# Kernel optimization log

Measured on AMD Instinct MI355X. Metric: run time of the kernel, lower is better.

The kernel has to match this reference:

```python
import jax, jax.numpy as jnp
import numpy as np

N_NODES = 200_000
N_EDGES = 6_400_000
N_GRAPHS = 512
F_IN = 92   # CGCNN atom feature dim
WIDTH = 10  # hard-coded config.width in GCNSimple
F_OUT = 1   # output_features


def setup_inputs() -> dict:
    key = jax.random.key(0)
    ks = jax.random.split(key, 10)
    atom_features = jax.random.normal(ks[0], (N_NODES, F_IN), dtype=jnp.float32)
    r = jax.random.normal(ks[1], (N_EDGES, 3), dtype=jnp.float32)
    W_emb = jax.random.normal(ks[2], (F_IN, WIDTH), dtype=jnp.float32) * 0.1
    b_emb = jax.random.normal(ks[3], (WIDTH,), dtype=jnp.float32) * 0.1
    W1 = jax.random.normal(ks[4], (WIDTH, WIDTH), dtype=jnp.float32) * 0.3
    b1 = jax.random.normal(ks[5], (WIDTH,), dtype=jnp.float32) * 0.1
    W2 = jax.random.normal(ks[6], (WIDTH, F_OUT), dtype=jnp.float32) * 0.3
    b2 = jax.random.normal(ks[7], (F_OUT,), dtype=jnp.float32) * 0.1
    src = jax.random.randint(ks[8], (N_EDGES,), 0, N_NODES, dtype=jnp.int32)
    dst = jax.random.randint(ks[9], (N_EDGES,), 0, N_NODES, dtype=jnp.int32)
    graph_ids = jnp.sort(jax.random.randint(jax.random.fold_in(key, 99), (N_NODES,), 0, N_GRAPHS, dtype=jnp.int32))
    return {
        "atom_features": atom_features, "r": r,
        "W_emb": W_emb, "b_emb": b_emb, "W1": W1, "b1": b1, "W2": W2, "b2": b2,
        "src": src, "dst": dst, "graph_ids": graph_ids, "num_graphs": N_GRAPHS,
    }


def reference(atom_features, r, W_emb, b_emb, W1, b1, W2, b2, src, dst, graph_ids, num_graphs):
    n = atom_features.shape[0]
    dt = atom_features.dtype
    # edge weights: exp(-||r||^2 / lengthscale^2), lengthscale = 1
    ew = jnp.exp(-jnp.sum(r * r, axis=1))  # [E]

    # unweighted degrees (DGL GraphConv norm='both' ignores edge_weight in norm)
    out_deg = jnp.clip(jnp.zeros(n, dt).at[src].add(1.0), 1.0)
    in_deg = jnp.clip(jnp.zeros(n, dt).at[dst].add(1.0), 1.0)
    inv_sqrt_out = out_deg ** -0.5
    inv_sqrt_in = in_deg ** -0.5

    def gconv(x, W, b, mm_first):
        # DGL GraphConv, norm='both': scale by src deg, weighted-sum aggregate,
        # scale by dst deg; weight applied before aggregation iff in > out.
        x = x * inv_sqrt_out[:, None]
        if mm_first:
            x = x @ W
        msg = x[src] * ew[:, None]                      # [E, d] gather
        agg = jax.ops.segment_sum(msg, dst, num_segments=n)  # [N, d] scatter-add
        if not mm_first:
            agg = agg @ W
        return agg * inv_sqrt_in[:, None] + b

    h = atom_features @ W_emb + b_emb                  # atom embedding [N, 10]
    x = jax.nn.relu(gconv(h, W1, b1, mm_first=False))  # 10 -> 10 (in == out: aggregate first)
    x = gconv(x, W2, b2, mm_first=True)                # 10 -> 1  (in > out: mm first)

    # AvgPooling: mean node feature per graph
    counts = jax.ops.segment_sum(jnp.ones(n, dt), graph_ids, num_segments=num_graphs)
    pooled = jax.ops.segment_sum(x, graph_ids, num_segments=num_graphs) / counts[:, None]
    return jnp.squeeze(pooled)  # [num_graphs]
```

## Files before the change

kernel.cpp:

```cpp
#include <hip/hip_runtime.h>
#include <math.h>

#define NNODES  200000
#define NEDGES  6400000
#define NGRAPHS 512
#define FIN     92
#define WID     10
#define HPAD    16
#define NBLK    ((NNODES + 255) / 256)

#define LBITS   10
#define LSIZE   1024
#define LMASK   (LSIZE - 1)
#define NB      196
#define SUBSH   7
#define SUBN    128
#define NSUB    1563
#define NSUBP   1608
#define PBLK    1280
#define EPB     (NEDGES / PBLK)
#define TILE    1250
#define NTILE   (EPB / TILE)
#define CELLS   (2 * NB)
#define CNT_N   (CELLS * PBLK)
#define SBLKS   (CNT_N / 256)
#define REF_GRID (NB * 8)

#define CHBITS  14
#define NCHK    13
#define SKEYS   (SUBN * NCHK)
#define SKPAD   1792
#define SKPT    7
#define SMAX    5120

#define LPN     8
#define LPNSH   3
#define NPB     (256 / LPN)
#define AGG_BLKS (NNODES / NPB)

__global__ void k_part_count(const int* __restrict__ src,
                             const int* __restrict__ dst,
                             int* __restrict__ cnt,
                             int* __restrict__ subcnt) {
    __shared__ int hSub[NSUB];
    __shared__ int hS[NB];
    int tid = threadIdx.x, k = blockIdx.x;
    for (int i = tid; i < NSUB; i += 256) hSub[i] = 0;
    if (tid < NB) hS[tid] = 0;
    __syncthreads();
    int base = k * EPB;
    for (int i = tid; i < EPB; i += 256) {
        int e = base + i;
        atomicAdd(&hSub[dst[e] >> SUBSH], 1);
        atomicAdd(&hS[src[e] >> LBITS], 1);
    }
    __syncthreads();
    if (tid < NB) {
        int s = 0;
        int b0 = tid * 8;
#pragma unroll
        for (int j = 0; j < 8; j++) {
            int ix = b0 + j;
            if (ix < NSUB) s += hSub[ix];
        }
        cnt[tid * PBLK + k] = s;
        cnt[(NB + tid) * PBLK + k] = hS[tid];
    }
    for (int i = tid; i < NSUB; i += 256) {
        int v = hSub[i];
        if (v) atomicAdd(&subcnt[i], v);
    }
}

__global__ void k_scan_partial(const int* __restrict__ cnt,
                               int* __restrict__ partial) {
    __shared__ int sdata[256];
    int tid = threadIdx.x;
    sdata[tid] = cnt[blockIdx.x * 256 + tid];
    __syncthreads();
    for (int s = 128; s > 0; s >>= 1) {
        if (tid < s) sdata[tid] += sdata[tid + s];
        __syncthreads();
    }
    if (tid == 0) partial[blockIdx.x] = sdata[0];
}

__global__ void k_scan_top(int* __restrict__ partial) {
    __shared__ int buf[1024];
    __shared__ int carry_s;
    if (threadIdx.x == 0) carry_s = 0;
    __syncthreads();
    for (int base = 0; base < SBLKS; base += 1024) {
        int i = base + threadIdx.x;
        int c = carry_s;
        int orig = (i < SBLKS) ? partial[i] : 0;
        buf[threadIdx.x] = orig;
        __syncthreads();
        for (int off = 1; off < 1024; off <<= 1) {
            int t = (threadIdx.x >= off) ? buf[threadIdx.x - off] : 0;
            __syncthreads();
            buf[threadIdx.x] += t;
            __syncthreads();
        }
        if (i < SBLKS) partial[i] = buf[threadIdx.x] - orig + c;
        __syncthreads();
        if (threadIdx.x == 0) carry_s = c + buf[1023];
        __syncthreads();
    }
}

__global__ void k_scan_apply(int* __restrict__ cnt,
                             const int* __restrict__ partial) {
    __shared__ int buf[256];
    int tid = threadIdx.x;
    int i = blockIdx.x * 256 + tid;
    int v = cnt[i];
    buf[tid] = v;
    __syncthreads();
    for (int off = 1; off < 256; off <<= 1) {
        int t = (tid >= off) ? buf[tid - off] : 0;
        __syncthreads();
        buf[tid] += t;
        __syncthreads();
    }
    cnt[i] = buf[tid] - v + partial[blockIdx.x];
}

__global__ void k_subscan(int* __restrict__ subcnt,
                          int* __restrict__ subcur) {
    __shared__ int sbuf[256];
    int tid = threadIdx.x;
    int vals[SKPT];
    int sum = 0;
#pragma unroll
    for (int j = 0; j < SKPT; j++) {
        int c = tid * SKPT + j;
        int v = (c < NSUB) ? subcnt[c] : 0;
        vals[j] = v;
        sum += v;
    }
    sbuf[tid] = sum;
    __syncthreads();
    for (int off = 1; off < 256; off <<= 1) {
        int t = (tid >= off) ? sbuf[tid - off] : 0;
        __syncthreads();
        sbuf[tid] += t;
        __syncthreads();
    }
    int run = sbuf[tid] - sum;
#pragma unroll
    for (int j = 0; j < SKPT; j++) {
        int c = tid * SKPT + j;
        if (c < NSUB) {
            subcnt[c] = run;
            subcur[c] = run;
            run += vals[j];
        }
    }
    if (tid == 0) subcnt[NSUB] = NEDGES;
}

__global__ void k_part_scatter(const float* __restrict__ r,
                               const int* __restrict__ src,
                               const int* __restrict__ dst,
                               const int* __restrict__ cnt,
                               float2* __restrict__ dstpart,
                               unsigned short* __restrict__ srcpart) {
    __shared__ int curD[NB], curS[NB];
    __shared__ int hD[NB], hS[NB];
    __shared__ int baseD[NB], baseS[NB];
    __shared__ int segD[NB], segS[NB];
    __shared__ int wsum[4];
    __shared__ float stW[TILE];
    __shared__ int   stK[TILE];
    __shared__ int   ddD[TILE];
    __shared__ unsigned short stS[TILE];
    __shared__ int   ddS[TILE];

    int tid = threadIdx.x, k = blockIdx.x;
    int lane = tid & 63, wv = tid >> 6;
    if (tid < NB) {
        curD[tid] = cnt[tid * PBLK + k];
        curS[tid] = cnt[(NB + tid) * PBLK + k] - NEDGES;
    }
    __syncthreads();

    int base = k * EPB;
    for (int t = 0; t < NTILE; t++) {
        int tbase = base + t * TILE;
        if (tid < NB) { hD[tid] = 0; hS[tid] = 0; }
        __syncthreads();
        for (int i = tid; i < TILE; i += 256) {
            int e = tbase + i;
            atomicAdd(&hD[dst[e] >> LBITS], 1);
            atomicAdd(&hS[src[e] >> LBITS], 1);
        }
        __syncthreads();
        {
            int v = (tid < NB) ? hD[tid] : 0;
            int x = v;
#pragma unroll
            for (int off = 1; off < 64; off <<= 1) {
                int tv = __shfl_up(x, off, 64);
                if (lane >= off) x += tv;
            }
            if (lane == 63) wsum[wv] = x;
            __syncthreads();
            if (tid == 0) {
                int a = 0;
#pragma unroll
                for (int wvi = 0; wvi < 4; wvi++) { int tv = wsum[wvi]; wsum[wvi] = a; a += tv; }
            }
            __syncthreads();
            int excl = x - v + wsum[wv];
            if (tid < NB) {
                baseD[tid] = excl;
                segD[tid] = curD[tid];
                curD[tid] += v;
                hD[tid] = excl;
            }
        }
        __syncthreads();
        {
            int v = (tid < NB) ? hS[tid] : 0;
            int x = v;
#pragma unroll
            for (int off = 1; off < 64; off <<= 1) {
                int tv = __shfl_up(x, off, 64);
                if (lane >= off) x += tv;
            }
            if (lane == 63) wsum[wv] = x;
            __syncthreads();
            if (tid == 0) {
                int a = 0;
#pragma unroll
                for (int wvi = 0; wvi < 4; wvi++) { int tv = wsum[wvi]; wsum[wvi] = a; a += tv; }
            }
            __syncthreads();
            int excl = x - v + wsum[wv];
            if (tid < NB) {
                baseS[tid] = excl;
                segS[tid] = curS[tid];
                curS[tid] += v;
                hS[tid] = excl;
            }
        }
        __syncthreads();
        for (int i = tid; i < TILE; i += 256) {
            int e = tbase + i;
            int s = src[e], d = dst[e];
            float x = r[3 * e + 0];
            float y = r[3 * e + 1];
            float z = r[3 * e + 2];
            float w = expf(-(x * x + y * y + z * z));
            int cd = d >> LBITS;
            int idx = atomicAdd(&hD[cd], 1);
            stW[idx] = w;
            stK[idx] = (s << LBITS) | (d & LMASK);
            ddD[idx] = segD[cd] + (idx - baseD[cd]);
            int cs = s >> LBITS;
            int ids = atomicAdd(&hS[cs], 1);
            stS[ids] = (unsigned short)(s & LMASK);
            ddS[ids] = segS[cs] + (ids - baseS[cs]);
        }
        __syncthreads();
        for (int i = tid; i < TILE; i += 256) {
            dstpart[ddD[i]] = make_float2(stW[i], __int_as_float(stK[i]));
            srcpart[ddS[i]] = stS[i];
        }
        __syncthreads();
    }
}

__global__ void k_bucket_odeg(const unsigned short* __restrict__ srcpart,
                              const int* __restrict__ cnt,
                              float* __restrict__ inv_out) {
    __shared__ int hist[LSIZE];
    int tid = threadIdx.x, b = blockIdx.x;
    int bstart = cnt[(NB + b) * PBLK] - NEDGES;
    int bend = (b == NB - 1) ? NEDGES : (cnt[(NB + b + 1) * PBLK] - NEDGES);
    for (int l = tid; l < LSIZE; l += 256) hist[l] = 0;
    __syncthreads();
    for (int p = bstart + tid; p < bend; p += 256)
        atomicAdd(&hist[srcpart[p]], 1);
    __syncthreads();
    for (int l = tid; l < LSIZE; l += 256) {
        int n = (b << LBITS) + l;
        if (n < NNODES) {
            int c = hist[l];
            inv_out[n] = rsqrtf((float)(c < 1 ? 1 : c));
        }
    }
}

__global__ void k_refine(const float2* __restrict__ dstpart,
                         const int* __restrict__ cnt,
                         int* __restrict__ subcur,
                         float2* __restrict__ dstfine) {
    int p = blockIdx.x >> 3;
    int q = blockIdx.x & 7;
    int bstart = cnt[p * PBLK];
    int bend = (p == NB - 1) ? NEDGES : cnt[(p + 1) * PBLK];
    int sz = bend - bstart;
    int qs = bstart + (int)(((long long)sz * q) >> 3);
    int qe = bstart + (int)(((long long)sz * (q + 1)) >> 3);
    int lane = threadIdx.x & 63;
    int wv = threadIdx.x >> 6;

    for (int base = qs + wv * 64; base < qe; base += 256) {
        int i = base + lane;
        bool act = (i < qe);
        float2 rec = make_float2(0.0f, 0.0f);
        if (act) rec = dstpart[i];
        unsigned pk = __float_as_uint(rec.y);
        int s3 = (pk >> SUBSH) & 7;
        unsigned long long b0 = __ballot(s3 & 1);
        unsigned long long b1 = __ballot(s3 & 2);
        unsigned long long b2 = __ballot(s3 & 4);
        unsigned long long am = __ballot(act);
        unsigned long long M = ((s3 & 1) ? b0 : ~b0)
                             & ((s3 & 2) ? b1 : ~b1)
                             & ((s3 & 4) ? b2 : ~b2) & am;
        if (act) {
            int cj = __popcll(M);
            int rank = __popcll(M & ((1ull << lane) - 1ull));
            int leader = __ffsll((unsigned long long)M) - 1;
            int gb = 0;
            if (lane == leader) gb = atomicAdd(&subcur[p * 8 + s3], cj);
            gb = __shfl(gb, leader, 64);
            dstfine[gb + rank] = rec;
        }
    }
}

__global__ void k_bucket_csr(float2* __restrict__ data,
                             const int* __restrict__ subscan,
                             int* __restrict__ row_ptr,
                             float* __restrict__ inv_in) {
    __shared__ int hist[SKPAD];
    __shared__ int sbuf[256];
    __shared__ float2 stout[SMAX];
    int tid = threadIdx.x;
    int sub = blockIdx.x;
    int substart = subscan[sub];
    int subend = subscan[sub + 1];
    int sz = subend - substart;

    for (int j = tid; j < SKPAD; j += 256) hist[j] = 0;
    __syncthreads();
    for (int p = substart + tid; p < subend; p += 256) {
        unsigned pk = __float_as_uint(data[p].y);
        atomicAdd(&hist[(pk & 127u) * NCHK + (pk >> 24)], 1);
    }
    __syncthreads();
    int kb = tid * SKPT;
    int sum = 0;
#pragma unroll
    for (int j = 0; j < SKPT; j++) sum += hist[kb + j];
    sbuf[tid] = sum;
    __syncthreads();
    for (int off = 1; off < 256; off <<= 1) {
        int tv = (tid >= off) ? sbuf[tid - off] : 0;
        __syncthreads();
        sbuf[tid] += tv;
        __syncthreads();
    }
    int run = sbuf[tid] - sum + substart;
#pragma unroll
    for (int j = 0; j < SKPT; j++) {
        int c = hist[kb + j];
        hist[kb + j] = run;
        run += c;
    }
    __syncthreads();
    if (tid < SUBN) {
        int l = tid;
        int rs = hist[l * NCHK];
        int re = (l == SUBN - 1) ? subend : hist[(l + 1) * NCHK];
        int n = (sub << SUBSH) + l;
        if (n < NNODES) {
            row_ptr[n] = rs;
            int c = re - rs;
            inv_in[n] = rsqrtf((float)(c < 1 ? 1 : c));
        }
    }
    __syncthreads();
    if (sz <= SMAX) {
        for (int p = substart + tid; p < subend; p += 256) {
            float2 rec = data[p];
            unsigned pk = __float_as_uint(rec.y);
            int pos = atomicAdd(&hist[(pk & 127u) * NCHK + (pk >> 24)], 1);
            stout[pos - substart] = make_float2(rec.x, __int_as_float((int)(pk >> LBITS)));
        }
        __syncthreads();
        for (int i = tid; i < sz; i += 256)
            data[substart + i] = stout[i];
    } else {
        for (int p = substart + tid; p < subend; p += 256) {
            float2 rec = data[p];
            unsigned pk = __float_as_uint(rec.y);
            int pos = atomicAdd(&hist[(pk & 127u) * NCHK + (pk >> 24)], 1);
            data[pos] = make_float2(rec.x, __int_as_float((int)(pk >> LBITS)));
        }
    }
}

__global__ void k_embed(const float* __restrict__ A,
                        const float* __restrict__ Wemb,
                        const float* __restrict__ bemb,
                        const float* __restrict__ inv_out,
                        float* __restrict__ hs) {
    __shared__ float sW[FIN * WID];
    __shared__ float sb[WID];
    for (int i = threadIdx.x; i < FIN * WID; i += blockDim.x) sW[i] = Wemb[i];
    if (threadIdx.x < WID) sb[threadIdx.x] = bemb[threadIdx.x];
    __syncthreads();

    int n = blockIdx.x * blockDim.x + threadIdx.x;
    if (n >= NNODES) return;

    float acc[WID];
#pragma unroll
    for (int k = 0; k < WID; k++) acc[k] = sb[k];

    const float4* row4 = reinterpret_cast<const float4*>(A + (size_t)n * FIN);
#pragma unroll
    for (int f4 = 0; f4 < FIN / 4; f4++) {
        float4 v = row4[f4];
        int f = f4 * 4;
#pragma unroll
        for (int k = 0; k < WID; k++) acc[k] += v.x * sW[(f + 0) * WID + k];
#pragma unroll
        for (int k = 0; k < WID; k++) acc[k] += v.y * sW[(f + 1) * WID + k];
#pragma unroll
        for (int k = 0; k < WID; k++) acc[k] += v.z * sW[(f + 2) * WID + k];
#pragma unroll
        for (int k = 0; k < WID; k++) acc[k] += v.w * sW[(f + 3) * WID + k];
    }

    float sc = inv_out[n];
    float* out = hs + (size_t)n * HPAD;
    float4 o0 = make_float4(acc[0] * sc, acc[1] * sc, acc[2] * sc, acc[3] * sc);
    float4 o1 = make_float4(acc[4] * sc, acc[5] * sc, acc[6] * sc, acc[7] * sc);
    float2 o2 = make_float2(acc[8] * sc, acc[9] * sc);
    *reinterpret_cast<float4*>(out + 0) = o0;
    *reinterpret_cast<float4*>(out + 4) = o1;
    *reinterpret_cast<float2*>(out + 8) = o2;
}

__global__ void k_agg1(const float2* __restrict__ csr,
                       const int* __restrict__ row_ptr,
                       const float* __restrict__ hs,
                       const float* __restrict__ W1,
                       const float* __restrict__ b1,
                       const float* __restrict__ W2,
                       const float* __restrict__ inv_in,
                       const float* __restrict__ inv_out,
                       float* __restrict__ sproj) {
    __shared__ float sW1[WID * WID];
    __shared__ float sb1[WID];
    __shared__ float sW2[WID];
    for (int i = threadIdx.x; i < WID * WID; i += blockDim.x) sW1[i] = W1[i];
    if (threadIdx.x < WID) {
        sb1[threadIdx.x] = b1[threadIdx.x];
        sW2[threadIdx.x] = W2[threadIdx.x];
    }
    __syncthreads();

    int tid = threadIdx.x;
    int sub = tid & (LPN - 1);
    int n = blockIdx.x * NPB + (tid >> LPNSH);

    int start = row_ptr[n];
    int end = (n == NNODES - 1) ? NEDGES : row_ptr[n + 1];

    float acc[WID];
#pragma unroll
    for (int k = 0; k < WID; k++) acc[k] = 0.0f;

    int p = start + sub;
    for (int c = 0; c < NCHK; c++) {
        int slim = (c + 1) << CHBITS;
        while (p < end) {
            float2 c2 = csr[p];
            int s = __float_as_int(c2.y);
            if (s >= slim) break;
            float w = c2.x;
            const float* hrow = hs + (size_t)s * HPAD;
            float4 a = *reinterpret_cast<const float4*>(hrow + 0);
            float4 b = *reinterpret_cast<const float4*>(hrow + 4);
            float2 cc = *reinterpret_cast<const float2*>(hrow + 8);
            acc[0] += w * a.x; acc[1] += w * a.y; acc[2] += w * a.z; acc[3] += w * a.w;
            acc[4] += w * b.x; acc[5] += w * b.y; acc[6] += w * b.z; acc[7] += w * b.w;
            acc[8] += w * cc.x; acc[9] += w * cc.y;
            p += LPN;
        }
        __syncthreads();
    }
    for (; p < end; p += LPN) {
        float2 c2 = csr[p];
        float w = c2.x;
        int s = __float_as_int(c2.y);
        const float* hrow = hs + (size_t)s * HPAD;
        float4 a = *reinterpret_cast<const float4*>(hrow + 0);
        float4 b = *reinterpret_cast<const float4*>(hrow + 4);
        float2 cc = *reinterpret_cast<const float2*>(hrow + 8);
        acc[0] += w * a.x; acc[1] += w * a.y; acc[2] += w * a.z; acc[3] += w * a.w;
        acc[4] += w * b.x; acc[5] += w * b.y; acc[6] += w * b.z; acc[7] += w * b.w;
        acc[8] += w * cc.x; acc[9] += w * cc.y;
    }

#pragma unroll
    for (int m = 1; m < LPN; m <<= 1) {
#pragma unroll
        for (int k = 0; k < WID; k++) acc[k] += __shfl_xor(acc[k], m, 64);
    }

    float ii = inv_in[n];
    float dot = 0.0f;
#pragma unroll
    for (int j = 0; j < WID; j++) {
        float y = 0.0f;
#pragma unroll
        for (int k = 0; k < WID; k++) y += acc[k] * sW1[k * WID + j];
        y = y * ii + sb1[j];
        y = y > 0.0f ? y : 0.0f;
        dot += y * sW2[j];
    }
    if (sub == 0) sproj[n] = dot * inv_out[n];
}

__global__ void k_agg2_pool(const float2* __restrict__ csr,
                            const int* __restrict__ row_ptr,
                            const float* __restrict__ sproj,
                            const float* __restrict__ inv_in,
                            const float* __restrict__ b2,
                            const int* __restrict__ graph_ids,
                            float* __restrict__ pooled) {
    int tid = threadIdx.x;
    int lane = tid & 63;
    int sub = tid & (LPN - 1);
    int n = blockIdx.x * NPB + (tid >> LPNSH);

    int start = row_ptr[n];
    int end = (n == NNODES - 1) ? NEDGES : row_ptr[n + 1];
    float sum = 0.0f;
    for (int p = start + sub; p < end; p += LPN) {
        float2 c2 = csr[p];
        sum += c2.x * sproj[__float_as_int(c2.y)];
    }
#pragma unroll
    for (int m = 1; m < LPN; m <<= 1) sum += __shfl_xor(sum, m, 64);

    float v = sum * inv_in[n] + b2[0];
    int g = graph_ids[n];

#pragma unroll
    for (int off = LPN; off < 64; off <<= 1) {
        float vv = __shfl_down(v, off, 64);
        int gg = __shfl_down(g, off, 64);
        if (lane + off < 64 && gg == g) v += vv;
    }
    int gprev = __shfl_up(g, LPN, 64);
    bool head = (sub == 0) && (lane < LPN || gprev != g);
    if (head) atomicAdd(&pooled[g], v);
}

__global__ void k_final(const float* __restrict__ pooled,
                        const int* __restrict__ gids,
                        float* __restrict__ out) {
    int g = blockIdx.x * blockDim.x + threadIdx.x;
    if (g >= NGRAPHS) return;
    int lo = 0, hi = NNODES;
    while (lo < hi) { int m = (lo + hi) >> 1; if (gids[m] < g) lo = m + 1; else hi = m; }
    int first = lo;
    hi = NNODES;
    while (lo < hi) { int m = (lo + hi) >> 1; if (gids[m] < g + 1) lo = m + 1; else hi = m; }
    int cnt = lo - first;
    out[g] = pooled[g] / (float)(cnt > 0 ? cnt : 1);
}

extern "C" void kernel_launch(void* const* d_in, const int* in_sizes, int n_in,
                              void* d_out, int out_size, void* d_ws, size_t ws_size,
                              hipStream_t stream) {
    const float* atom = (const float*)d_in[0];
    const float* r    = (const float*)d_in[1];
    const float* Wemb = (const float*)d_in[2];
    const float* bemb = (const float*)d_in[3];
    const float* W1   = (const float*)d_in[4];
    const float* b1   = (const float*)d_in[5];
    const float* W2   = (const float*)d_in[6];
    const float* b2   = (const float*)d_in[7];
    const int*   src  = (const int*)d_in[8];
    const int*   dst  = (const int*)d_in[9];
    const int*   gids = (const int*)d_in[10];
    float* out = (float*)d_out;

    char* w = (char*)d_ws;
    float* pooled  = (float*)w;  w += (size_t)NGRAPHS * 4;
    int*   subscan = (int*)w;    w += (size_t)NSUBP * 4;
    int*   subcur  = (int*)w;    w += (size_t)NSUBP * 4;
    int*   cnt     = (int*)w;    w += (size_t)CNT_N * 4;
    int*   partial = (int*)w;    w += (size_t)((SBLKS + 3) & ~3) * 4;
    int*   row_ptr = (int*)w;    w += (size_t)((NNODES + 4) & ~3) * 4;
    float* inv_in  = (float*)w;  w += (size_t)NNODES * 4;
    float* inv_out = (float*)w;  w += (size_t)NNODES * 4;
    float* sproj   = (float*)w;  w += (size_t)NNODES * 4;
    float* hs      = (float*)w;  w += (size_t)NNODES * HPAD * 4;
    float2* dstpart = (float2*)w; w += (size_t)NEDGES * 8;
    float2* csrbuf  = (float2*)w; w += (size_t)NEDGES * 8;
    unsigned short* srcpart = (unsigned short*)csrbuf;

    hipMemsetAsync(pooled, 0, (size_t)NGRAPHS * 4, stream);
    hipMemsetAsync(subscan, 0, (size_t)NSUBP * 4, stream);

    const int B = 256;

    k_part_count<<<PBLK, B, 0, stream>>>(src, dst, cnt, subscan);
    k_scan_partial<<<SBLKS, B, 0, stream>>>(cnt, partial);
    k_scan_top<<<1, 1024, 0, stream>>>(partial);
    k_scan_apply<<<SBLKS, B, 0, stream>>>(cnt, partial);
    k_subscan<<<1, B, 0, stream>>>(subscan, subcur);
    k_part_scatter<<<PBLK, B, 0, stream>>>(r, src, dst, cnt, dstpart, srcpart);
    k_bucket_odeg<<<NB, B, 0, stream>>>(srcpart, cnt, inv_out);
    k_refine<<<REF_GRID, B, 0, stream>>>(dstpart, cnt, subcur, csrbuf);
    k_bucket_csr<<<NSUB, B, 0, stream>>>(csrbuf, subscan, row_ptr, inv_in);
    k_embed<<<NBLK, B, 0, stream>>>(atom, Wemb, bemb, inv_out, hs);
    k_agg1<<<AGG_BLKS, B, 0, stream>>>(csrbuf, row_ptr, hs, W1, b1, W2, inv_in, inv_out, sproj);
    k_agg2_pool<<<AGG_BLKS, B, 0, stream>>>(csrbuf, row_ptr, sproj, inv_in, b2, gids, pooled);
    k_final<<<(NGRAPHS + B - 1) / B, B, 0, stream>>>(pooled, gids, out);
}
```

Before: 694.8 us.

## Add grid-wide soft barrier between source chunks in first aggregation

The first aggregation kernel becomes a persistent-style launch of 512 blocks of 1024 threads, with two lanes per node instead of eight. Between source-index chunks, blocks synchronise through a hierarchical atomic barrier (eight counters feeding one global counter) with a bounded spin. The aim is to keep every block on the same slice of the embedding table at once, so gathers stay cache-resident across the whole GPU instead of only within a block. The spin is capped, so correctness does not depend on all blocks being co-resident, but spinning costs time, and fewer lanes per node lengthens each node's serial loop.

```diff
diff --git a/kernel.cpp b/kernel.cpp
--- a/kernel.cpp
+++ b/kernel.cpp
@@ -32,6 +32,11 @@
 #define SKPAD   1792
 #define SKPT    7
 #define SMAX    5120
+
+#define AGG_THR  1024
+#define AGG_GRID 512
+#define GPB      (AGG_THR / 2)
+#define SPIN_MAX 1536
 
 #define LPN     8
 #define LPNSH   3
@@ -448,31 +453,37 @@
     *reinterpret_cast<float2*>(out + 8) = o2;
 }
 
-__global__ void k_agg1(const float2* __restrict__ csr,
-                       const int* __restrict__ row_ptr,
-                       const float* __restrict__ hs,
-                       const float* __restrict__ W1,
-                       const float* __restrict__ b1,
-                       const float* __restrict__ W2,
-                       const float* __restrict__ inv_in,
-                       const float* __restrict__ inv_out,
-                       float* __restrict__ sproj) {
+__global__ __launch_bounds__(AGG_THR, 8)
+void k_agg1(const float2* __restrict__ csr,
+            const int* __restrict__ row_ptr,
+            const float* __restrict__ hs,
+            const float* __restrict__ W1,
+            const float* __restrict__ b1,
+            const float* __restrict__ W2,
+            const float* __restrict__ inv_in,
+            const float* __restrict__ inv_out,
+            int* __restrict__ bar8,
+            int* __restrict__ bar,
+            float* __restrict__ sproj) {
     __shared__ float sW1[WID * WID];
     __shared__ float sb1[WID];
     __shared__ float sW2[WID];
-    for (int i = threadIdx.x; i < WID * WID; i += blockDim.x) sW1[i] = W1[i];
-    if (threadIdx.x < WID) {
-        sb1[threadIdx.x] = b1[threadIdx.x];
-        sW2[threadIdx.x] = W2[threadIdx.x];
-    }
-    __syncthreads();
-
     int tid = threadIdx.x;
-    int sub = tid & (LPN - 1);
-    int n = blockIdx.x * NPB + (tid >> LPNSH);
-
-    int start = row_ptr[n];
-    int end = (n == NNODES - 1) ? NEDGES : row_ptr[n + 1];
+    for (int i = tid; i < WID * WID; i += AGG_THR) sW1[i] = W1[i];
+    if (tid < WID) {
+        sb1[tid] = b1[tid];
+        sW2[tid] = W2[tid];
+    }
+    __syncthreads();
+
+    int sub = tid & 1;
+    int n = blockIdx.x * GPB + (tid >> 1);
+    bool valid = (n < NNODES);
+    int start = 0, end = 0;
+    if (valid) {
+        start = row_ptr[n];
+        end = (n == NNODES - 1) ? NEDGES : row_ptr[n + 1];
+    }
 
     float acc[WID];
 #pragma unroll
@@ -493,11 +504,23 @@
             acc[0] += w * a.x; acc[1] += w * a.y; acc[2] += w * a.z; acc[3] += w * a.w;
             acc[4] += w * b.x; acc[5] += w * b.y; acc[6] += w * b.z; acc[7] += w * b.w;
             acc[8] += w * cc.x; acc[9] += w * cc.y;
-            p += LPN;
-        }
-        __syncthreads();
-    }
-    for (; p < end; p += LPN) {
+            p += 2;
+        }
+        if (c < NCHK - 1) {
+            __syncthreads();
+            if (tid == 0) {
+                int a = atomicAdd(&bar8[c * 8 + (blockIdx.x & 7)], 1);
+                if (a == (AGG_GRID / 8) - 1) atomicAdd(&bar[c], 1);
+                int t = 0;
+                while (__hip_atomic_load(&bar[c], __ATOMIC_RELAXED,
+                                         __HIP_MEMORY_SCOPE_AGENT) < 8 &&
+                       ++t < SPIN_MAX)
+                    __builtin_amdgcn_s_sleep(2);
+            }
+            __syncthreads();
+        }
+    }
+    for (; p < end; p += 2) {
         float2 c2 = csr[p];
         float w = c2.x;
         int s = __float_as_int(c2.y);
@@ -511,11 +534,9 @@
     }
 
 #pragma unroll
-    for (int m = 1; m < LPN; m <<= 1) {
-#pragma unroll
-        for (int k = 0; k < WID; k++) acc[k] += __shfl_xor(acc[k], m, 64);
-    }
-
+    for (int k = 0; k < WID; k++) acc[k] += __shfl_xor(acc[k], 1, 64);
+
+    if (!valid || sub != 0) return;
     float ii = inv_in[n];
     float dot = 0.0f;
 #pragma unroll
@@ -527,7 +548,7 @@
         y = y > 0.0f ? y : 0.0f;
         dot += y * sW2[j];
     }
-    if (sub == 0) sproj[n] = dot * inv_out[n];
+    sproj[n] = dot * inv_out[n];
 }
 
 __global__ void k_agg2_pool(const float2* __restrict__ csr,
@@ -598,6 +619,7 @@
 
     char* w = (char*)d_ws;
     float* pooled  = (float*)w;  w += (size_t)NGRAPHS * 4;
+    int*   barmem  = (int*)w;    w += (size_t)128 * 4;
     int*   subscan = (int*)w;    w += (size_t)NSUBP * 4;
     int*   subcur  = (int*)w;    w += (size_t)NSUBP * 4;
     int*   cnt     = (int*)w;    w += (size_t)CNT_N * 4;
@@ -611,7 +633,11 @@
     float2* csrbuf  = (float2*)w; w += (size_t)NEDGES * 8;
     unsigned short* srcpart = (unsigned short*)csrbuf;
 
+    int* bar8 = barmem;
+    int* bar  = barmem + 104;
+
     hipMemsetAsync(pooled, 0, (size_t)NGRAPHS * 4, stream);
+    hipMemsetAsync(barmem, 0, (size_t)128 * 4, stream);
     hipMemsetAsync(subscan, 0, (size_t)NSUBP * 4, stream);
 
     const int B = 256;
@@ -626,7 +652,8 @@
     k_refine<<<REF_GRID, B, 0, stream>>>(dstpart, cnt, subcur, csrbuf);
     k_bucket_csr<<<NSUB, B, 0, stream>>>(csrbuf, subscan, row_ptr, inv_in);
     k_embed<<<NBLK, B, 0, stream>>>(atom, Wemb, bemb, inv_out, hs);
-    k_agg1<<<AGG_BLKS, B, 0, stream>>>(csrbuf, row_ptr, hs, W1, b1, W2, inv_in, inv_out, sproj);
+    k_agg1<<<AGG_GRID, AGG_THR, 0, stream>>>(csrbuf, row_ptr, hs, W1, b1, W2,
+                                             inv_in, inv_out, bar8, bar, sproj);
     k_agg2_pool<<<AGG_BLKS, B, 0, stream>>>(csrbuf, row_ptr, sproj, inv_in, b2, gids, pooled);
     k_final<<<(NGRAPHS + B - 1) / B, B, 0, stream>>>(pooled, gids, out);
 }
```

Result: slower. 754.7 us (+8.6%).

## Fuse subscan into scan_top, finalize pooling via last-block ticket, drop chunked agg1 loop

Applied to the files above, without the earlier changes.

Merges the sub-bucket prefix scan into the single-block top-level scan kernel and folds the final pooling division into k_agg2_pool using a last-block-done atomic ticket, removing two kernel launches. It also removes the chunked, block-synchronized traversal in k_agg1 (which ordered source accesses by chunk for cache locality) in favour of a plain strided loop, and lets non-leader lanes exit early. The ticket pattern depends on threadfence ordering and adds a counter to the memset, and dropping the chunking may reduce L2 locality for the hs gathers.

```diff
diff --git a/kernel.cpp b/kernel.cpp
--- a/kernel.cpp
+++ b/kernel.cpp
@@ -85,28 +85,47 @@
     if (tid == 0) partial[blockIdx.x] = sdata[0];
 }
 
-__global__ void k_scan_top(int* __restrict__ partial) {
+__global__ void k_scan_top(int* __restrict__ partial,
+                           int* __restrict__ subcnt,
+                           int* __restrict__ subcur) {
     __shared__ int buf[1024];
     __shared__ int carry_s;
-    if (threadIdx.x == 0) carry_s = 0;
+    int tid = threadIdx.x;
+    if (tid == 0) carry_s = 0;
     __syncthreads();
     for (int base = 0; base < SBLKS; base += 1024) {
-        int i = base + threadIdx.x;
+        int i = base + tid;
         int c = carry_s;
         int orig = (i < SBLKS) ? partial[i] : 0;
-        buf[threadIdx.x] = orig;
+        buf[tid] = orig;
         __syncthreads();
         for (int off = 1; off < 1024; off <<= 1) {
-            int t = (threadIdx.x >= off) ? buf[threadIdx.x - off] : 0;
+            int t = (tid >= off) ? buf[tid - off] : 0;
             __syncthreads();
-            buf[threadIdx.x] += t;
+            buf[tid] += t;
             __syncthreads();
         }
-        if (i < SBLKS) partial[i] = buf[threadIdx.x] - orig + c;
-        __syncthreads();
-        if (threadIdx.x == 0) carry_s = c + buf[1023];
-        __syncthreads();
-    }
+        if (i < SBLKS) partial[i] = buf[tid] - orig + c;
+        __syncthreads();
+        if (tid == 0) carry_s = c + buf[1023];
+        __syncthreads();
+    }
+    int c0 = tid * 2, c1 = tid * 2 + 1;
+    int v0 = (c0 < NSUB) ? subcnt[c0] : 0;
+    int v1 = (c1 < NSUB) ? subcnt[c1] : 0;
+    int sum = v0 + v1;
+    buf[tid] = sum;
+    __syncthreads();
+    for (int off = 1; off < 1024; off <<= 1) {
+        int t = (tid >= off) ? buf[tid - off] : 0;
+        __syncthreads();
+        buf[tid] += t;
+        __syncthreads();
+    }
+    int run = buf[tid] - sum;
+    if (c0 < NSUB) { subcnt[c0] = run; subcur[c0] = run; run += v0; }
+    if (c1 < NSUB) { subcnt[c1] = run; subcur[c1] = run; }
+    if (tid == 0) subcnt[NSUB] = NEDGES;
 }
 
 __global__ void k_scan_apply(int* __restrict__ cnt,
@@ -124,40 +143,6 @@
         __syncthreads();
     }
     cnt[i] = buf[tid] - v + partial[blockIdx.x];
-}
-
-__global__ void k_subscan(int* __restrict__ subcnt,
-                          int* __restrict__ subcur) {
-    __shared__ int sbuf[256];
-    int tid = threadIdx.x;
-    int vals[SKPT];
-    int sum = 0;
-#pragma unroll
-    for (int j = 0; j < SKPT; j++) {
-        int c = tid * SKPT + j;
-        int v = (c < NSUB) ? subcnt[c] : 0;
-        vals[j] = v;
-        sum += v;
-    }
-    sbuf[tid] = sum;
-    __syncthreads();
-    for (int off = 1; off < 256; off <<= 1) {
-        int t = (tid >= off) ? sbuf[tid - off] : 0;
-        __syncthreads();
-        sbuf[tid] += t;
-        __syncthreads();
-    }
-    int run = sbuf[tid] - sum;
-#pragma unroll
-    for (int j = 0; j < SKPT; j++) {
-        int c = tid * SKPT + j;
-        if (c < NSUB) {
-            subcnt[c] = run;
-            subcur[c] = run;
-            run += vals[j];
-        }
-    }
-    if (tid == 0) subcnt[NSUB] = NEDGES;
 }
 
 __global__ void k_part_scatter(const float* __restrict__ r,
@@ -478,26 +463,7 @@
 #pragma unroll
     for (int k = 0; k < WID; k++) acc[k] = 0.0f;
 
-    int p = start + sub;
-    for (int c = 0; c < NCHK; c++) {
-        int slim = (c + 1) << CHBITS;
-        while (p < end) {
-            float2 c2 = csr[p];
-            int s = __float_as_int(c2.y);
-            if (s >= slim) break;
-            float w = c2.x;
-            const float* hrow = hs + (size_t)s * HPAD;
-            float4 a = *reinterpret_cast<const float4*>(hrow + 0);
-            float4 b = *reinterpret_cast<const float4*>(hrow + 4);
-            float2 cc = *reinterpret_cast<const float2*>(hrow + 8);
-            acc[0] += w * a.x; acc[1] += w * a.y; acc[2] += w * a.z; acc[3] += w * a.w;
-            acc[4] += w * b.x; acc[5] += w * b.y; acc[6] += w * b.z; acc[7] += w * b.w;
-            acc[8] += w * cc.x; acc[9] += w * cc.y;
-            p += LPN;
-        }
-        __syncthreads();
-    }
-    for (; p < end; p += LPN) {
+    for (int p = start + sub; p < end; p += LPN) {
         float2 c2 = csr[p];
         float w = c2.x;
         int s = __float_as_int(c2.y);
@@ -516,6 +482,7 @@
         for (int k = 0; k < WID; k++) acc[k] += __shfl_xor(acc[k], m, 64);
     }
 
+    if (sub != 0) return;
     float ii = inv_in[n];
     float dot = 0.0f;
 #pragma unroll
@@ -527,7 +494,7 @@
         y = y > 0.0f ? y : 0.0f;
         dot += y * sW2[j];
     }
-    if (sub == 0) sproj[n] = dot * inv_out[n];
+    sproj[n] = dot * inv_out[n];
 }
 
 __global__ void k_agg2_pool(const float2* __restrict__ csr,
@@ -536,7 +503,10 @@
                             const float* __restrict__ inv_in,
                             const float* __restrict__ b2,
                             const int* __restrict__ graph_ids,
-                            float* __restrict__ pooled) {
+                            float* __restrict__ pooled,
+                            int* __restrict__ done,
+                            float* __restrict__ out) {
+    __shared__ int ticket_s;
     int tid = threadIdx.x;
     int lane = tid & 63;
     int sub = tid & (LPN - 1);
@@ -564,20 +534,24 @@
     int gprev = __shfl_up(g, LPN, 64);
     bool head = (sub == 0) && (lane < LPN || gprev != g);
     if (head) atomicAdd(&pooled[g], v);
-}
-
-__global__ void k_final(const float* __restrict__ pooled,
-                        const int* __restrict__ gids,
-                        float* __restrict__ out) {
-    int g = blockIdx.x * blockDim.x + threadIdx.x;
-    if (g >= NGRAPHS) return;
-    int lo = 0, hi = NNODES;
-    while (lo < hi) { int m = (lo + hi) >> 1; if (gids[m] < g) lo = m + 1; else hi = m; }
-    int first = lo;
-    hi = NNODES;
-    while (lo < hi) { int m = (lo + hi) >> 1; if (gids[m] < g + 1) lo = m + 1; else hi = m; }
-    int cnt = lo - first;
-    out[g] = pooled[g] / (float)(cnt > 0 ? cnt : 1);
+
+    __threadfence();
+    __syncthreads();
+    if (tid == 0) ticket_s = atomicAdd(done, 1);
+    __syncthreads();
+    if (ticket_s == AGG_BLKS - 1) {
+        for (int g2 = tid; g2 < NGRAPHS; g2 += 256) {
+            float pv = __hip_atomic_load(&pooled[g2], __ATOMIC_RELAXED,
+                                         __HIP_MEMORY_SCOPE_AGENT);
+            int lo = 0, hi = NNODES;
+            while (lo < hi) { int m = (lo + hi) >> 1; if (graph_ids[m] < g2) lo = m + 1; else hi = m; }
+            int first = lo;
+            hi = NNODES;
+            while (lo < hi) { int m = (lo + hi) >> 1; if (graph_ids[m] < g2 + 1) lo = m + 1; else hi = m; }
+            int cnt = lo - first;
+            out[g2] = pv / (float)(cnt > 0 ? cnt : 1);
+        }
+    }
 }
 
 extern "C" void kernel_launch(void* const* d_in, const int* in_sizes, int n_in,
@@ -598,6 +572,7 @@
 
     char* w = (char*)d_ws;
     float* pooled  = (float*)w;  w += (size_t)NGRAPHS * 4;
+    int*   done    = (int*)w;    w += (size_t)16 * 4;
     int*   subscan = (int*)w;    w += (size_t)NSUBP * 4;
     int*   subcur  = (int*)w;    w += (size_t)NSUBP * 4;
     int*   cnt     = (int*)w;    w += (size_t)CNT_N * 4;
@@ -611,22 +586,21 @@
     float2* csrbuf  = (float2*)w; w += (size_t)NEDGES * 8;
     unsigned short* srcpart = (unsigned short*)csrbuf;
 
-    hipMemsetAsync(pooled, 0, (size_t)NGRAPHS * 4, stream);
+    hipMemsetAsync(pooled, 0, (size_t)NGRAPHS * 4 + 64, stream);
     hipMemsetAsync(subscan, 0, (size_t)NSUBP * 4, stream);
 
     const int B = 256;
 
     k_part_count<<<PBLK, B, 0, stream>>>(src, dst, cnt, subscan);
     k_scan_partial<<<SBLKS, B, 0, stream>>>(cnt, partial);
-    k_scan_top<<<1, 1024, 0, stream>>>(partial);
+    k_scan_top<<<1, 1024, 0, stream>>>(partial, subscan, subcur);
     k_scan_apply<<<SBLKS, B, 0, stream>>>(cnt, partial);
-    k_subscan<<<1, B, 0, stream>>>(subscan, subcur);
     k_part_scatter<<<PBLK, B, 0, stream>>>(r, src, dst, cnt, dstpart, srcpart);
     k_bucket_odeg<<<NB, B, 0, stream>>>(srcpart, cnt, inv_out);
     k_refine<<<REF_GRID, B, 0, stream>>>(dstpart, cnt, subcur, csrbuf);
     k_bucket_csr<<<NSUB, B, 0, stream>>>(csrbuf, subscan, row_ptr, inv_in);
     k_embed<<<NBLK, B, 0, stream>>>(atom, Wemb, bemb, inv_out, hs);
     k_agg1<<<AGG_BLKS, B, 0, stream>>>(csrbuf, row_ptr, hs, W1, b1, W2, inv_in, inv_out, sproj);
-    k_agg2_pool<<<AGG_BLKS, B, 0, stream>>>(csrbuf, row_ptr, sproj, inv_in, b2, gids, pooled);
-    k_final<<<(NGRAPHS + B - 1) / B, B, 0, stream>>>(pooled, gids, out);
-}
+    k_agg2_pool<<<AGG_BLKS, B, 0, stream>>>(csrbuf, row_ptr, sproj, inv_in, b2, gids,
+                                            pooled, done, out);
+}
```

After: 1.130 ms. +62.6%, slower.
